# Kernel optimization log

Hardware: AMD Instinct MI355X
Metric: run time of the kernel (lower is better)

## Reference

```python
import jax, jax.numpy as jnp
import numpy as np
import math

H = 8          # n_head
MAX_POS = 48   # block_size / max_positions
MAX_PART = 16  # max_particles


def _rel_bias(table, L, max_len):
    # table: (2*max_len-1, H). Equivalent to the tile/view trick in
    # SimpleRelativePositionalBias: bias[h, i, j] = b[j - i + L - 1, h]
    b = table[max_len - L: max_len + L - 1]          # (2L-1, H)
    idx = jnp.arange(L)
    rel = idx[None, :] - idx[:, None] + (L - 1)      # (L, L) in [0, 2L-2]
    return jnp.transpose(b[rel], (2, 0, 1))          # (H, L, L)


def setup_inputs() -> dict:
    key = jax.random.key(0)
    ks = jax.random.split(key, 7)
    B, N, T, C = 16, 16, 48, 512
    s = 0.02
    return {
        "x": jax.random.normal(ks[0], (B, N, T, C), jnp.float32),
        "Wq": jax.random.normal(ks[1], (C, C), jnp.float32) * s,
        "Wk": jax.random.normal(ks[2], (C, C), jnp.float32) * s,
        "Wv": jax.random.normal(ks[3], (C, C), jnp.float32) * s,
        "Wo": jax.random.normal(ks[4], (C, C), jnp.float32) * s,
        "rel_pos_bias": jax.random.normal(ks[5], (2 * MAX_POS - 1, H), jnp.float32) * s,
        "particle_rel_pos_bias": jax.random.normal(ks[6], (2 * MAX_PART - 1, H), jnp.float32) * s,
    }


def reference(x, Wq, Wk, Wv, Wo, rel_pos_bias, particle_rel_pos_bias):
    B, N, T, C = x.shape
    hd = C // H
    L = N * T
    xf = x.reshape(B, L, C)
    # (B, H, L, hd) each; Linear with no bias
    q = (xf @ Wq).reshape(B, L, H, hd).transpose(0, 2, 1, 3)
    k = (xf @ Wk).reshape(B, L, H, hd).transpose(0, 2, 1, 3)
    v = (xf @ Wv).reshape(B, L, H, hd).transpose(0, 2, 1, 3)

    att = jnp.einsum('bhqd,bhkd->bhqk', q, k) * (1.0 / math.sqrt(hd))
    att = att.reshape(B, H, N, T, N, T)

    bias_t = _rel_bias(rel_pos_bias, T, MAX_POS).reshape(1, H, 1, T, 1, T)
    bias_p = _rel_bias(particle_rel_pos_bias, N, MAX_PART).reshape(1, H, N, 1, N, 1)
    att = att + bias_t + bias_p

    # causal over the time axes only (all particles at allowed times visible)
    causal = jnp.tril(jnp.ones((T, T), dtype=bool))
    att = jnp.where(causal[None, None, None, :, None, :], att, -jnp.inf)

    att = jax.nn.softmax(att.reshape(B, H, L, L), axis=-1)
    y = att @ v                                      # (B, H, L, hd)
    y = y.transpose(0, 2, 1, 3).reshape(B, L, C) @ Wo
    return y.reshape(B, N, T, C)
```

## Files before the change

### kernel.cpp

```cpp
#include <hip/hip_runtime.h>
#include <hip/hip_bf16.h>
#include <math.h>

#define B_  16
#define N_  16
#define T_  48
#define C_  512
#define H_  8
#define HD_ 64
#define L_  768
#define BL_ 12288

typedef __attribute__((ext_vector_type(8))) short b16x8;
typedef __attribute__((ext_vector_type(4))) float f32x4;
typedef __attribute__((ext_vector_type(2))) unsigned int u32x2;

__device__ __forceinline__ short f2b(float f) {
  __hip_bfloat16 h = __float2bfloat16(f);
  return *reinterpret_cast<short*>(&h);
}
__device__ __forceinline__ unsigned cvt_pk_bf16(float a, float b) {
  unsigned d;
  asm("v_cvt_pk_bf16_f32 %0, %1, %2" : "=v"(d) : "v"(a), "v"(b));
  return d;
}
__device__ __forceinline__ float ex2(float x) {
  float d;
  asm("v_exp_f32 %0, %1" : "=v"(d) : "v"(x));
  return d;
}
__device__ __forceinline__ void gload16(const void* g, void* l) {
  __builtin_amdgcn_global_load_lds(
      (const __attribute__((address_space(1))) void*)g,
      (__attribute__((address_space(3))) void*)l, 16, 0, 0);
}

__global__ __launch_bounds__(256) void prep_kernel(
    const float* __restrict__ x,
    const float* __restrict__ Wq, const float* __restrict__ Wk,
    const float* __restrict__ Wv, const float* __restrict__ Wo,
    short* __restrict__ xb, short* __restrict__ WT)
{
  __shared__ float tile[32][33];
  int blk = blockIdx.x;
  int tid = threadIdx.x;
  if (blk < 3072) {
    int i = blk * 256 + tid;
    const float4* src = (const float4*)(x + (size_t)i * 8);
    float4 a = src[0], b = src[1];
    short tmp[8] = {f2b(a.x), f2b(a.y), f2b(a.z), f2b(a.w),
                    f2b(b.x), f2b(b.y), f2b(b.z), f2b(b.w)};
    *(b16x8*)(xb + (size_t)i * 8) = *(b16x8*)tmp;
  } else {
    int idx = blk - 3072;
    int mat = idx >> 8, rem = idx & 255;
    const float* W = (mat == 0) ? Wq : (mat == 1) ? Wk : (mat == 2) ? Wv : Wo;
    float scale = (mat == 0) ? 0.18033688f : 1.0f;
    int k0 = (rem >> 4) * 32, n0 = (rem & 15) * 32;
    int tx = tid & 31, ty = tid >> 5;
    for (int i = ty; i < 32; i += 8) tile[i][tx] = W[(size_t)(k0 + i) * 512 + n0 + tx];
    __syncthreads();
    short* dst = WT + (size_t)mat * 262144;
    for (int i = ty; i < 32; i += 8)
      dst[(size_t)(n0 + i) * 512 + k0 + tx] = f2b(tile[tx][i] * scale);
  }
}

__global__ __launch_bounds__(256) void qkv_kernel(
    const short* __restrict__ xb, const short* __restrict__ WT,
    short* __restrict__ q2, short* __restrict__ k2, short* __restrict__ vT2)
{
  __shared__ __align__(16) short smem[16384];
  int tid = threadIdx.x;
  int w = tid >> 6, lane = tid & 63, n16 = lane & 15, quad = lane >> 4;
  int bm = blockIdx.x, bn = blockIdx.y;
  int mat = bn >> 2;
  int ncol0 = (bn & 3) * 128;
  const short* Wt = WT + (size_t)mat * 262144;
  int bq = bm / 6;
  int rr0 = (bm % 6) * 128;

  f32x4 zero4 = {0.f, 0.f, 0.f, 0.f};
  f32x4 acc[4][4];
  #pragma unroll
  for (int mt = 0; mt < 4; ++mt)
    #pragma unroll
    for (int nt = 0; nt < 4; ++nt) acc[mt][nt] = zero4;

  const short* gA[2];
  const short* gB[2];
  #pragma unroll
  for (int i = 0; i < 2; ++i) {
    int r16 = w + 4 * i;
    int rr = rr0 + r16 * 16 + (lane >> 2);
    int pt = rr >> 4, pn = rr & 15;
    gA[i] = xb + ((size_t)bq * 768 + pn * 48 + pt) * 512 + (lane & 3) * 8;
    gB[i] = Wt + (size_t)(ncol0 + r16 * 16 + (lane >> 2)) * 512 + (lane & 3) * 8;
  }
  int ldsoff = (w) * 512 + lane * 8;

  auto stage = [&](int buf, int kt) {
    short* As = smem + buf * 8192;
    short* Bs = As + 4096;
    #pragma unroll
    for (int i = 0; i < 2; ++i) {
      gload16(gA[i] + kt * 32, As + i * 2048 + ldsoff);
      gload16(gB[i] + kt * 32, Bs + i * 2048 + ldsoff);
    }
  };

  int wm = (w >> 1) * 64, wn = (w & 1) * 64;
  stage(0, 0);
  __syncthreads();
  int buf = 0;
  for (int kt = 0; kt < 16; ++kt) {
    if (kt < 15) stage(buf ^ 1, kt + 1);
    const short (*As)[32] = (const short(*)[32])(smem + buf * 8192);
    const short (*Bs)[32] = (const short(*)[32])(smem + buf * 8192 + 4096);
    b16x8 af[4], bf[4];
    #pragma unroll
    for (int mt = 0; mt < 4; ++mt) af[mt] = *(const b16x8*)&As[wm + mt * 16 + n16][quad * 8];
    #pragma unroll
    for (int nt = 0; nt < 4; ++nt) bf[nt] = *(const b16x8*)&Bs[wn + nt * 16 + n16][quad * 8];
    #pragma unroll
    for (int mt = 0; mt < 4; ++mt)
      #pragma unroll
      for (int nt = 0; nt < 4; ++nt)
        acc[mt][nt] = __builtin_amdgcn_mfma_f32_16x16x32_bf16(af[mt], bf[nt], acc[mt][nt], 0, 0, 0);
    __syncthreads();
    buf ^= 1;
  }

  short (*Ls)[136] = (short(*)[136])smem;
  for (int c = 0; c < 4; ++c) {
    __syncthreads();
    if ((w >> 1) == (c >> 1)) {
      int mtb = (c & 1) * 2;
      #pragma unroll
      for (int mi = 0; mi < 2; ++mi) {
        #pragma unroll
        for (int nt = 0; nt < 4; ++nt)
          #pragma unroll
          for (int r = 0; r < 4; ++r)
            Ls[mi * 16 + quad * 4 + r][wn + nt * 16 + n16] = f2b(acc[mtb + mi][nt][r]);
      }
    }
    __syncthreads();
    int rrc = rr0 + c * 32;
    if (mat != 2) {
      short* dst = (mat == 0) ? q2 : k2;
      int row = tid >> 3, c0 = (tid & 7) * 16;
      int hhg = (ncol0 + c0) >> 6, d0 = (ncol0 + c0) & 63;
      short* dp = dst + ((size_t)(bq * 8 + hhg) * 768 + rrc + row) * 64 + d0;
      *(b16x8*)dp       = *(b16x8*)&Ls[row][c0];
      *(b16x8*)(dp + 8) = *(b16x8*)&Ls[row][c0 + 8];
    } else {
      int cp = tid & 63, r8 = (tid >> 6) * 8;
      int c0 = 2 * cp;
      int hhg = (ncol0 + c0) >> 6, d0 = (ncol0 + c0) & 63;
      short t0[8], t1[8];
      #pragma unroll
      for (int j = 0; j < 8; ++j) { t0[j] = Ls[r8 + j][c0]; t1[j] = Ls[r8 + j][c0 + 1]; }
      short* dp = vT2 + ((size_t)(bq * 8 + hhg) * 64 + d0) * 768 + rrc + r8;
      *(b16x8*)dp         = *(b16x8*)t0;
      *(b16x8*)(dp + 768) = *(b16x8*)t1;
    }
  }
}

__global__ __launch_bounds__(128, 3) void attn_kernel(
    const short* __restrict__ q2, const short* __restrict__ k2,
    const short* __restrict__ vT2,
    const float* __restrict__ relT, const float* __restrict__ relP,
    short* __restrict__ yatt)
{
  __shared__ __align__(16) short KV[2][4096];
  __shared__ float btL[2][96];

  const float LOG2E = 1.44269504f;
  int tid = threadIdx.x;
  int wv = tid >> 6, lane = tid & 63, n16 = lane & 15, quad = lane >> 4;
  int blk = blockIdx.x;
  int h = blk & 7;
  int g = blk >> 3;
  int pg = g % 12, b = g / 12;
  int pair = pg * 2 + wv;
  int qtA = pair, qtB = 47 - pair;
  int nA = pg + 1;
  int nB = 24 - pg;

  btL[wv][lane] = relT[(lane < 95 ? lane : 94) * 8 + h] * LOG2E;
  if (lane < 32) btL[wv][64 + lane] = relT[((64 + lane) < 95 ? 64 + lane : 94) * 8 + h] * LOG2E;

  float bpT[4];
  #pragma unroll
  for (int r = 0; r < 4; ++r)
    bpT[r] = relP[(quad * 4 + r - n16 + 15) * 8 + h] * LOG2E;

  size_t bh = (size_t)(b * 8 + h);
  const short* qb = q2 + bh * 49152;
  const short* kb = k2 + bh * 49152;
  const short* vb = vT2 + bh * 49152;

  b16x8 qA0 = *(const b16x8*)(qb + (qtA * 16 + n16) * 64 + quad * 8);
  b16x8 qA1 = *(const b16x8*)(qb + (qtA * 16 + n16) * 64 + quad * 8 + 32);
  b16x8 qB0 = *(const b16x8*)(qb + (qtB * 16 + n16) * 64 + quad * 8);
  b16x8 qB1 = *(const b16x8*)(qb + (qtB * 16 + n16) * 64 + quad * 8 + 32);

  f32x4 zero4 = {0.f, 0.f, 0.f, 0.f};
  f32x4 oA[4], oB[4];
  float psA = 0.f, psB = 0.f;
  #pragma unroll
  for (int nt = 0; nt < 4; ++nt) { oA[nt] = zero4; oB[nt] = zero4; }

  int krow = tid >> 3, kc8 = tid & 7;
  int vd   = tid >> 2, vkc = tid & 3;
  int kdst = (kc8 < 4 ? 0 : 1024) + krow * 32 + (kc8 & 3) * 8;
  int vdst = 2048 + vd * 32 + vkc * 8;
  b16x8 s0, s1, s2, s3;
  auto LOADR = [&](int kt2) {
    const short* kq = kb + (size_t)(kt2 * 32 + krow) * 64 + kc8 * 8;
    s0 = *(const b16x8*)kq;
    s1 = *(const b16x8*)(kq + 16 * 64);
    const short* vq = vb + (size_t)vd * 768 + kt2 * 32 + vkc * 8;
    s2 = *(const b16x8*)vq;
    s3 = *(const b16x8*)(vq + (size_t)32 * 768);
  };
  auto WRITE = [&](int buf) {
    short* p = KV[buf];
    *(b16x8*)(p + kdst)       = s0;
    *(b16x8*)(p + kdst + 512) = s1;
    *(b16x8*)(p + vdst)        = s2;
    *(b16x8*)(p + vdst + 1024) = s3;
  };

  auto exp_pack = [&](const f32x4& s0v, const f32x4& s1v, float bt0, float bt1,
                      float& ps) -> b16x8 {
    float e00 = ex2(s0v[0] + bt0 + bpT[0]);
    float e01 = ex2(s0v[1] + bt0 + bpT[1]);
    float e02 = ex2(s0v[2] + bt0 + bpT[2]);
    float e03 = ex2(s0v[3] + bt0 + bpT[3]);
    float e10 = ex2(s1v[0] + bt1 + bpT[0]);
    float e11 = ex2(s1v[1] + bt1 + bpT[1]);
    float e12 = ex2(s1v[2] + bt1 + bpT[2]);
    float e13 = ex2(s1v[3] + bt1 + bpT[3]);
    ps += ((e00 + e01) + (e02 + e03)) + ((e10 + e11) + (e12 + e13));
    unsigned p0 = cvt_pk_bf16(e00, e01);
    unsigned p1 = cvt_pk_bf16(e02, e03);
    unsigned p2 = cvt_pk_bf16(e10, e11);
    unsigned p3 = cvt_pk_bf16(e12, e13);
    u32x2 a02 = __builtin_amdgcn_permlane32_swap(p0, p2, false, false);
    u32x2 z02 = __builtin_amdgcn_permlane16_swap(a02.x, a02.y, false, false);
    u32x2 a13 = __builtin_amdgcn_permlane32_swap(p1, p3, false, false);
    u32x2 z13 = __builtin_amdgcn_permlane16_swap(a13.x, a13.y, false, false);
    union { unsigned u[4]; b16x8 v; } r;
    r.u[0] = z02.x;
    r.u[1] = z13.x;
    r.u[2] = z02.y;
    r.u[3] = z13.y;
    return r.v;
  };

  LOADR(0);
  WRITE(0);
  __syncthreads();

  int buf = 0;
  for (int kt2 = 0; kt2 < nB; ++kt2) {
    bool more = (kt2 + 1 < nB);
    if (more) LOADR(kt2 + 1);

    const short* p = KV[buf];
    b16x8 kf0 = *(const b16x8*)(p + n16 * 32 + quad * 8);
    b16x8 kf1 = *(const b16x8*)(p + 1024 + n16 * 32 + quad * 8);
    b16x8 kf2 = *(const b16x8*)(p + (16 + n16) * 32 + quad * 8);
    b16x8 kf3 = *(const b16x8*)(p + 1024 + (16 + n16) * 32 + quad * 8);
    b16x8 vf0 = *(const b16x8*)(p + 2048 + n16 * 32 + quad * 8);
    b16x8 vf1 = *(const b16x8*)(p + 2048 + (16 + n16) * 32 + quad * 8);
    b16x8 vf2 = *(const b16x8*)(p + 2048 + (32 + n16) * 32 + quad * 8);
    b16x8 vf3 = *(const b16x8*)(p + 2048 + (48 + n16) * 32 + quad * 8);

    int kt0 = kt2 * 2;
    bool doA = kt2 < nA;
    f32x4 sB0 = zero4, sB1 = zero4;
    sB0 = __builtin_amdgcn_mfma_f32_16x16x32_bf16(kf0, qB0, sB0, 0, 0, 0);
    sB0 = __builtin_amdgcn_mfma_f32_16x16x32_bf16(kf1, qB1, sB0, 0, 0, 0);
    sB1 = __builtin_amdgcn_mfma_f32_16x16x32_bf16(kf2, qB0, sB1, 0, 0, 0);
    sB1 = __builtin_amdgcn_mfma_f32_16x16x32_bf16(kf3, qB1, sB1, 0, 0, 0);
    f32x4 sA0 = zero4, sA1 = zero4;
    if (doA) {
      sA0 = __builtin_amdgcn_mfma_f32_16x16x32_bf16(kf0, qA0, sA0, 0, 0, 0);
      sA0 = __builtin_amdgcn_mfma_f32_16x16x32_bf16(kf1, qA1, sA0, 0, 0, 0);
      sA1 = __builtin_amdgcn_mfma_f32_16x16x32_bf16(kf2, qA0, sA1, 0, 0, 0);
      sA1 = __builtin_amdgcn_mfma_f32_16x16x32_bf16(kf3, qA1, sA1, 0, 0, 0);
    }
    float btB0 = (kt0 <= qtB) ? btL[wv][kt0 - qtB + 47] : -1e30f;
    float btB1 = (kt0 + 1 <= qtB) ? btL[wv][kt0 + 1 - qtB + 47] : -1e30f;
    b16x8 pfB = exp_pack(sB0, sB1, btB0, btB1, psB);
    oB[0] = __builtin_amdgcn_mfma_f32_16x16x32_bf16(pfB, vf0, oB[0], 0, 0, 0);
    oB[1] = __builtin_amdgcn_mfma_f32_16x16x32_bf16(pfB, vf1, oB[1], 0, 0, 0);
    oB[2] = __builtin_amdgcn_mfma_f32_16x16x32_bf16(pfB, vf2, oB[2], 0, 0, 0);
    oB[3] = __builtin_amdgcn_mfma_f32_16x16x32_bf16(pfB, vf3, oB[3], 0, 0, 0);
    if (doA) {
      float btA0 = (kt0 <= qtA) ? btL[wv][kt0 - qtA + 47] : -1e30f;
      float btA1 = (kt0 + 1 <= qtA) ? btL[wv][kt0 + 1 - qtA + 47] : -1e30f;
      b16x8 pfA = exp_pack(sA0, sA1, btA0, btA1, psA);
      oA[0] = __builtin_amdgcn_mfma_f32_16x16x32_bf16(pfA, vf0, oA[0], 0, 0, 0);
      oA[1] = __builtin_amdgcn_mfma_f32_16x16x32_bf16(pfA, vf1, oA[1], 0, 0, 0);
      oA[2] = __builtin_amdgcn_mfma_f32_16x16x32_bf16(pfA, vf2, oA[2], 0, 0, 0);
      oA[3] = __builtin_amdgcn_mfma_f32_16x16x32_bf16(pfA, vf3, oA[3], 0, 0, 0);
    }

    if (more) WRITE(buf ^ 1);
    __syncthreads();
    buf ^= 1;
  }

  psA += __shfl_xor(psA, 16); psA += __shfl_xor(psA, 32);
  psB += __shfl_xor(psB, 16); psB += __shfl_xor(psB, 32);
  float invA = 1.0f / psA, invB = 1.0f / psB;
  float pnA[4], pnB[4];
  #pragma unroll
  for (int r = 0; r < 4; ++r) {
    pnA[r] = __shfl(invA, quad * 4 + r);
    pnB[r] = __shfl(invB, quad * 4 + r);
  }

  #pragma unroll
  for (int nt = 0; nt < 4; ++nt) {
    int c = h * 64 + nt * 16 + n16;
    #pragma unroll
    for (int r = 0; r < 4; ++r) {
      int qn = quad * 4 + r;
      yatt[((size_t)b * 768 + qn * 48 + qtA) * 512 + c] = f2b(oA[nt][r] * pnA[r]);
      yatt[((size_t)b * 768 + qn * 48 + qtB) * 512 + c] = f2b(oB[nt][r] * pnB[r]);
    }
  }
}

__global__ __launch_bounds__(256) void proj_kernel(
    const short* __restrict__ yatt, const short* __restrict__ WT,
    float* __restrict__ out)
{
  __shared__ __align__(16) short smem[16384];
  int tid = threadIdx.x;
  int w = tid >> 6, lane = tid & 63, n16 = lane & 15, quad = lane >> 4;
  int row0 = blockIdx.x * 128;
  int ncol0 = blockIdx.y * 128;
  const short* Wt = WT + (size_t)3 * 262144;

  f32x4 zero4 = {0.f, 0.f, 0.f, 0.f};
  f32x4 acc[4][4];
  #pragma unroll
  for (int mt = 0; mt < 4; ++mt)
    #pragma unroll
    for (int nt = 0; nt < 4; ++nt) acc[mt][nt] = zero4;

  const short* gA[2];
  const short* gB[2];
  #pragma unroll
  for (int i = 0; i < 2; ++i) {
    int r16 = w + 4 * i;
    gA[i] = yatt + (size_t)(row0 + r16 * 16 + (lane >> 2)) * 512 + (lane & 3) * 8;
    gB[i] = Wt + (size_t)(ncol0 + r16 * 16 + (lane >> 2)) * 512 + (lane & 3) * 8;
  }
  int ldsoff = w * 512 + lane * 8;

  auto stage = [&](int buf, int kt) {
    short* As = smem + buf * 8192;
    short* Bs = As + 4096;
    #pragma unroll
    for (int i = 0; i < 2; ++i) {
      gload16(gA[i] + kt * 32, As + i * 2048 + ldsoff);
      gload16(gB[i] + kt * 32, Bs + i * 2048 + ldsoff);
    }
  };

  int wm = (w >> 1) * 64, wn = (w & 1) * 64;
  stage(0, 0);
  __syncthreads();
  int buf = 0;
  for (int kt = 0; kt < 16; ++kt) {
    if (kt < 15) stage(buf ^ 1, kt + 1);
    const short (*As)[32] = (const short(*)[32])(smem + buf * 8192);
    const short (*Bs)[32] = (const short(*)[32])(smem + buf * 8192 + 4096);
    b16x8 af[4], bf[4];
    #pragma unroll
    for (int mt = 0; mt < 4; ++mt) af[mt] = *(const b16x8*)&As[wm + mt * 16 + n16][quad * 8];
    #pragma unroll
    for (int nt = 0; nt < 4; ++nt) bf[nt] = *(const b16x8*)&Bs[wn + nt * 16 + n16][quad * 8];
    #pragma unroll
    for (int mt = 0; mt < 4; ++mt)
      #pragma unroll
      for (int nt = 0; nt < 4; ++nt)
        acc[mt][nt] = __builtin_amdgcn_mfma_f32_16x16x32_bf16(af[mt], bf[nt], acc[mt][nt], 0, 0, 0);
    __syncthreads();
    buf ^= 1;
  }

  #pragma unroll
  for (int mt = 0; mt < 4; ++mt) {
    int rowb = row0 + wm + mt * 16 + quad * 4;
    #pragma unroll
    for (int nt = 0; nt < 4; ++nt) {
      int colg = ncol0 + wn + nt * 16 + n16;
      #pragma unroll
      for (int r = 0; r < 4; ++r)
        out[(size_t)(rowb + r) * 512 + colg] = acc[mt][nt][r];
    }
  }
}

extern "C" void kernel_launch(void* const* d_in, const int* in_sizes, int n_in,
                              void* d_out, int out_size, void* d_ws, size_t ws_size,
                              hipStream_t stream) {
  const float* x    = (const float*)d_in[0];
  const float* Wq   = (const float*)d_in[1];
  const float* Wk   = (const float*)d_in[2];
  const float* Wv   = (const float*)d_in[3];
  const float* Wo   = (const float*)d_in[4];
  const float* relT = (const float*)d_in[5];
  const float* relP = (const float*)d_in[6];

  char* wsb = (char*)d_ws;
  const size_t SZ = (size_t)BL_ * C_ * 2;
  short* xb  = (short*)(wsb);
  short* WT  = (short*)(wsb + SZ);
  short* qb  = (short*)(wsb + SZ + 2097152);
  short* kb  = (short*)(wsb + 2 * SZ + 2097152);
  short* vTb = (short*)(wsb + 3 * SZ + 2097152);
  short* yat = (short*)(wsb + 4 * SZ + 2097152 + 4096);

  prep_kernel<<<dim3(4096), dim3(256), 0, stream>>>(x, Wq, Wk, Wv, Wo, xb, WT);
  qkv_kernel<<<dim3(96, 12), dim3(256), 0, stream>>>(xb, WT, qb, kb, vTb);
  attn_kernel<<<dim3(1536), dim3(128), 0, stream>>>(qb, kb, vTb, relT, relP, yat);
  proj_kernel<<<dim3(96, 4), dim3(256), 0, stream>>>(yat, WT, (float*)d_out);
}
```

Before: 157.4 us.

## Share K/V tiles across four waves per block and add MFMA priority hints

The attention kernel now runs 256-thread blocks with four waves, each handling a pair of query tiles, so every K/V tile staged in shared memory is reused by twice as many waves. Grid size is halved and each thread loads half as much per stage. Each wave skips compute once it passes its own causal limit, but it keeps joining the block barriers. s_setprio is placed around the MFMA groups to favour matrix issue. The trade-off is load imbalance inside a block, since waves with shorter causal ranges sit idle until the longest wave finishes.

```diff
diff --git a/kernel.cpp b/kernel.cpp
--- a/kernel.cpp
+++ b/kernel.cpp
@@ -168,29 +168,29 @@
   }
 }
 
-__global__ __launch_bounds__(128, 3) void attn_kernel(
+__global__ __launch_bounds__(256, 4) void attn_kernel(
     const short* __restrict__ q2, const short* __restrict__ k2,
     const short* __restrict__ vT2,
     const float* __restrict__ relT, const float* __restrict__ relP,
     short* __restrict__ yatt)
 {
   __shared__ __align__(16) short KV[2][4096];
-  __shared__ float btL[2][96];
+  __shared__ float btL[96];
 
   const float LOG2E = 1.44269504f;
   int tid = threadIdx.x;
-  int wv = tid >> 6, lane = tid & 63, n16 = lane & 15, quad = lane >> 4;
+  int w = tid >> 6, lane = tid & 63, n16 = lane & 15, quad = lane >> 4;
   int blk = blockIdx.x;
   int h = blk & 7;
   int g = blk >> 3;
-  int pg = g % 12, b = g / 12;
-  int pair = pg * 2 + wv;
-  int qtA = pair, qtB = 47 - pair;
-  int nA = pg + 1;
-  int nB = 24 - pg;
-
-  btL[wv][lane] = relT[(lane < 95 ? lane : 94) * 8 + h] * LOG2E;
-  if (lane < 32) btL[wv][64 + lane] = relT[((64 + lane) < 95 ? 64 + lane : 94) * 8 + h] * LOG2E;
+  int pgg = g % 6, b = g / 6;
+  int pairq = pgg * 4 + w;
+  int qtA = pairq, qtB = 47 - pairq;
+  int nAw = (qtA + 2) >> 1;
+  int nBw = (qtB + 2) >> 1;
+  int nBmax = 24 - 2 * pgg;
+
+  if (tid < 96) btL[tid] = relT[(tid < 95 ? tid : 94) * 8 + h] * LOG2E;
 
   float bpT[4];
   #pragma unroll
@@ -217,21 +217,14 @@
   int vd   = tid >> 2, vkc = tid & 3;
   int kdst = (kc8 < 4 ? 0 : 1024) + krow * 32 + (kc8 & 3) * 8;
   int vdst = 2048 + vd * 32 + vkc * 8;
-  b16x8 s0, s1, s2, s3;
+  b16x8 s0, s2;
   auto LOADR = [&](int kt2) {
-    const short* kq = kb + (size_t)(kt2 * 32 + krow) * 64 + kc8 * 8;
-    s0 = *(const b16x8*)kq;
-    s1 = *(const b16x8*)(kq + 16 * 64);
-    const short* vq = vb + (size_t)vd * 768 + kt2 * 32 + vkc * 8;
-    s2 = *(const b16x8*)vq;
-    s3 = *(const b16x8*)(vq + (size_t)32 * 768);
+    s0 = *(const b16x8*)(kb + (size_t)(kt2 * 32 + krow) * 64 + kc8 * 8);
+    s2 = *(const b16x8*)(vb + (size_t)vd * 768 + kt2 * 32 + vkc * 8);
   };
   auto WRITE = [&](int buf) {
-    short* p = KV[buf];
-    *(b16x8*)(p + kdst)       = s0;
-    *(b16x8*)(p + kdst + 512) = s1;
-    *(b16x8*)(p + vdst)        = s2;
-    *(b16x8*)(p + vdst + 1024) = s3;
+    *(b16x8*)(KV[buf] + kdst) = s0;
+    *(b16x8*)(KV[buf] + vdst) = s2;
   };
 
   auto exp_pack = [&](const f32x4& s0v, const f32x4& s1v, float bt0, float bt1,
@@ -266,49 +259,58 @@
   __syncthreads();
 
   int buf = 0;
-  for (int kt2 = 0; kt2 < nB; ++kt2) {
-    bool more = (kt2 + 1 < nB);
+  for (int kt2 = 0; kt2 < nBmax; ++kt2) {
+    bool more = (kt2 + 1 < nBmax);
     if (more) LOADR(kt2 + 1);
 
-    const short* p = KV[buf];
-    b16x8 kf0 = *(const b16x8*)(p + n16 * 32 + quad * 8);
-    b16x8 kf1 = *(const b16x8*)(p + 1024 + n16 * 32 + quad * 8);
-    b16x8 kf2 = *(const b16x8*)(p + (16 + n16) * 32 + quad * 8);
-    b16x8 kf3 = *(const b16x8*)(p + 1024 + (16 + n16) * 32 + quad * 8);
-    b16x8 vf0 = *(const b16x8*)(p + 2048 + n16 * 32 + quad * 8);
-    b16x8 vf1 = *(const b16x8*)(p + 2048 + (16 + n16) * 32 + quad * 8);
-    b16x8 vf2 = *(const b16x8*)(p + 2048 + (32 + n16) * 32 + quad * 8);
-    b16x8 vf3 = *(const b16x8*)(p + 2048 + (48 + n16) * 32 + quad * 8);
-
-    int kt0 = kt2 * 2;
-    bool doA = kt2 < nA;
-    f32x4 sB0 = zero4, sB1 = zero4;
-    sB0 = __builtin_amdgcn_mfma_f32_16x16x32_bf16(kf0, qB0, sB0, 0, 0, 0);
-    sB0 = __builtin_amdgcn_mfma_f32_16x16x32_bf16(kf1, qB1, sB0, 0, 0, 0);
-    sB1 = __builtin_amdgcn_mfma_f32_16x16x32_bf16(kf2, qB0, sB1, 0, 0, 0);
-    sB1 = __builtin_amdgcn_mfma_f32_16x16x32_bf16(kf3, qB1, sB1, 0, 0, 0);
-    f32x4 sA0 = zero4, sA1 = zero4;
-    if (doA) {
-      sA0 = __builtin_amdgcn_mfma_f32_16x16x32_bf16(kf0, qA0, sA0, 0, 0, 0);
-      sA0 = __builtin_amdgcn_mfma_f32_16x16x32_bf16(kf1, qA1, sA0, 0, 0, 0);
-      sA1 = __builtin_amdgcn_mfma_f32_16x16x32_bf16(kf2, qA0, sA1, 0, 0, 0);
-      sA1 = __builtin_amdgcn_mfma_f32_16x16x32_bf16(kf3, qA1, sA1, 0, 0, 0);
-    }
-    float btB0 = (kt0 <= qtB) ? btL[wv][kt0 - qtB + 47] : -1e30f;
-    float btB1 = (kt0 + 1 <= qtB) ? btL[wv][kt0 + 1 - qtB + 47] : -1e30f;
-    b16x8 pfB = exp_pack(sB0, sB1, btB0, btB1, psB);
-    oB[0] = __builtin_amdgcn_mfma_f32_16x16x32_bf16(pfB, vf0, oB[0], 0, 0, 0);
-    oB[1] = __builtin_amdgcn_mfma_f32_16x16x32_bf16(pfB, vf1, oB[1], 0, 0, 0);
-    oB[2] = __builtin_amdgcn_mfma_f32_16x16x32_bf16(pfB, vf2, oB[2], 0, 0, 0);
-    oB[3] = __builtin_amdgcn_mfma_f32_16x16x32_bf16(pfB, vf3, oB[3], 0, 0, 0);
-    if (doA) {
-      float btA0 = (kt0 <= qtA) ? btL[wv][kt0 - qtA + 47] : -1e30f;
-      float btA1 = (kt0 + 1 <= qtA) ? btL[wv][kt0 + 1 - qtA + 47] : -1e30f;
-      b16x8 pfA = exp_pack(sA0, sA1, btA0, btA1, psA);
-      oA[0] = __builtin_amdgcn_mfma_f32_16x16x32_bf16(pfA, vf0, oA[0], 0, 0, 0);
-      oA[1] = __builtin_amdgcn_mfma_f32_16x16x32_bf16(pfA, vf1, oA[1], 0, 0, 0);
-      oA[2] = __builtin_amdgcn_mfma_f32_16x16x32_bf16(pfA, vf2, oA[2], 0, 0, 0);
-      oA[3] = __builtin_amdgcn_mfma_f32_16x16x32_bf16(pfA, vf3, oA[3], 0, 0, 0);
+    bool doB = kt2 < nBw;
+    bool doA = kt2 < nAw;
+    if (doB) {
+      const short* p = KV[buf];
+      b16x8 kf0 = *(const b16x8*)(p + n16 * 32 + quad * 8);
+      b16x8 kf1 = *(const b16x8*)(p + 1024 + n16 * 32 + quad * 8);
+      b16x8 kf2 = *(const b16x8*)(p + (16 + n16) * 32 + quad * 8);
+      b16x8 kf3 = *(const b16x8*)(p + 1024 + (16 + n16) * 32 + quad * 8);
+      b16x8 vf0 = *(const b16x8*)(p + 2048 + n16 * 32 + quad * 8);
+      b16x8 vf1 = *(const b16x8*)(p + 2048 + (16 + n16) * 32 + quad * 8);
+      b16x8 vf2 = *(const b16x8*)(p + 2048 + (32 + n16) * 32 + quad * 8);
+      b16x8 vf3 = *(const b16x8*)(p + 2048 + (48 + n16) * 32 + quad * 8);
+
+      int kt0 = kt2 * 2;
+      __builtin_amdgcn_s_setprio(1);
+      f32x4 sB0 = zero4, sB1 = zero4;
+      sB0 = __builtin_amdgcn_mfma_f32_16x16x32_bf16(kf0, qB0, sB0, 0, 0, 0);
+      sB0 = __builtin_amdgcn_mfma_f32_16x16x32_bf16(kf1, qB1, sB0, 0, 0, 0);
+      sB1 = __builtin_amdgcn_mfma_f32_16x16x32_bf16(kf2, qB0, sB1, 0, 0, 0);
+      sB1 = __builtin_amdgcn_mfma_f32_16x16x32_bf16(kf3, qB1, sB1, 0, 0, 0);
+      f32x4 sA0 = zero4, sA1 = zero4;
+      if (doA) {
+        sA0 = __builtin_amdgcn_mfma_f32_16x16x32_bf16(kf0, qA0, sA0, 0, 0, 0);
+        sA0 = __builtin_amdgcn_mfma_f32_16x16x32_bf16(kf1, qA1, sA0, 0, 0, 0);
+        sA1 = __builtin_amdgcn_mfma_f32_16x16x32_bf16(kf2, qA0, sA1, 0, 0, 0);
+        sA1 = __builtin_amdgcn_mfma_f32_16x16x32_bf16(kf3, qA1, sA1, 0, 0, 0);
+      }
+      __builtin_amdgcn_s_setprio(0);
+      float btB0 = (kt0 <= qtB) ? btL[kt0 - qtB + 47] : -1e30f;
+      float btB1 = (kt0 + 1 <= qtB) ? btL[kt0 + 1 - qtB + 47] : -1e30f;
+      b16x8 pfB = exp_pack(sB0, sB1, btB0, btB1, psB);
+      __builtin_amdgcn_s_setprio(1);
+      oB[0] = __builtin_amdgcn_mfma_f32_16x16x32_bf16(pfB, vf0, oB[0], 0, 0, 0);
+      oB[1] = __builtin_amdgcn_mfma_f32_16x16x32_bf16(pfB, vf1, oB[1], 0, 0, 0);
+      oB[2] = __builtin_amdgcn_mfma_f32_16x16x32_bf16(pfB, vf2, oB[2], 0, 0, 0);
+      oB[3] = __builtin_amdgcn_mfma_f32_16x16x32_bf16(pfB, vf3, oB[3], 0, 0, 0);
+      __builtin_amdgcn_s_setprio(0);
+      if (doA) {
+        float btA0 = (kt0 <= qtA) ? btL[kt0 - qtA + 47] : -1e30f;
+        float btA1 = (kt0 + 1 <= qtA) ? btL[kt0 + 1 - qtA + 47] : -1e30f;
+        b16x8 pfA = exp_pack(sA0, sA1, btA0, btA1, psA);
+        __builtin_amdgcn_s_setprio(1);
+        oA[0] = __builtin_amdgcn_mfma_f32_16x16x32_bf16(pfA, vf0, oA[0], 0, 0, 0);
+        oA[1] = __builtin_amdgcn_mfma_f32_16x16x32_bf16(pfA, vf1, oA[1], 0, 0, 0);
+        oA[2] = __builtin_amdgcn_mfma_f32_16x16x32_bf16(pfA, vf2, oA[2], 0, 0, 0);
+        oA[3] = __builtin_amdgcn_mfma_f32_16x16x32_bf16(pfA, vf3, oA[3], 0, 0, 0);
+        __builtin_amdgcn_s_setprio(0);
+      }
     }
 
     if (more) WRITE(buf ^ 1);
@@ -433,6 +435,6 @@
 
   prep_kernel<<<dim3(4096), dim3(256), 0, stream>>>(x, Wq, Wk, Wv, Wo, xb, WT);
   qkv_kernel<<<dim3(96, 12), dim3(256), 0, stream>>>(xb, WT, qb, kb, vTb);
-  attn_kernel<<<dim3(1536), dim3(128), 0, stream>>>(qb, kb, vTb, relT, relP, yat);
+  attn_kernel<<<dim3(768), dim3(256), 0, stream>>>(qb, kb, vTb, relT, relP, yat);
   proj_kernel<<<dim3(96, 4), dim3(256), 0, stream>>>(yat, WT, (float*)d_out);
 }
```

New measurement: 156.9 us, median of 2. No clear change (-0.3%).

## Process four query time-tiles per wave to reuse K/V fragments

Applied to the files above, without the earlier changes.

Each wave in the attention kernel now handles two pairs of causally-balanced query time tiles (four in total) instead of one pair. Each K/V tile loaded into LDS and registers is therefore reused across more queries, and the grid shrinks from 1536 to 768 blocks. The relative-bias table is shared between the waves instead of duplicated per wave. In exchange it roughly doubles accumulator and Q register use, lowers the occupancy hint from 3 to 2, and within a block the two waves can now have unequal amounts of work.

```diff
diff --git a/kernel.cpp b/kernel.cpp
--- a/kernel.cpp
+++ b/kernel.cpp
@@ -168,29 +168,30 @@
   }
 }
 
-__global__ __launch_bounds__(128, 3) void attn_kernel(
+__global__ __launch_bounds__(128, 2) void attn_kernel(
     const short* __restrict__ q2, const short* __restrict__ k2,
     const short* __restrict__ vT2,
     const float* __restrict__ relT, const float* __restrict__ relP,
     short* __restrict__ yatt)
 {
   __shared__ __align__(16) short KV[2][4096];
-  __shared__ float btL[2][96];
+  __shared__ float btL[96];
 
   const float LOG2E = 1.44269504f;
   int tid = threadIdx.x;
-  int wv = tid >> 6, lane = tid & 63, n16 = lane & 15, quad = lane >> 4;
+  int w = tid >> 6, lane = tid & 63, n16 = lane & 15, quad = lane >> 4;
   int blk = blockIdx.x;
   int h = blk & 7;
   int g = blk >> 3;
-  int pg = g % 12, b = g / 12;
-  int pair = pg * 2 + wv;
-  int qtA = pair, qtB = 47 - pair;
-  int nA = pg + 1;
-  int nB = 24 - pg;
-
-  btL[wv][lane] = relT[(lane < 95 ? lane : 94) * 8 + h] * LOG2E;
-  if (lane < 32) btL[wv][64 + lane] = relT[((64 + lane) < 95 ? 64 + lane : 94) * 8 + h] * LOG2E;
+  int pgg = g % 6, b = g / 6;
+  int base = pgg * 4 + 2 * w;
+  int qtA0 = base,     qtB0 = 47 - base;
+  int qtA1 = base + 1, qtB1 = 46 - base;
+  int nA0 = (qtA0 + 2) >> 1, nA1 = (qtA1 + 2) >> 1;
+  int nB0 = (qtB0 + 2) >> 1, nB1 = (qtB1 + 2) >> 1;
+  int nBmax = 24 - 2 * pgg;
+
+  if (tid < 96) btL[tid] = relT[(tid < 95 ? tid : 94) * 8 + h] * LOG2E;
 
   float bpT[4];
   #pragma unroll
@@ -202,16 +203,22 @@
   const short* kb = k2 + bh * 49152;
   const short* vb = vT2 + bh * 49152;
 
-  b16x8 qA0 = *(const b16x8*)(qb + (qtA * 16 + n16) * 64 + quad * 8);
-  b16x8 qA1 = *(const b16x8*)(qb + (qtA * 16 + n16) * 64 + quad * 8 + 32);
-  b16x8 qB0 = *(const b16x8*)(qb + (qtB * 16 + n16) * 64 + quad * 8);
-  b16x8 qB1 = *(const b16x8*)(qb + (qtB * 16 + n16) * 64 + quad * 8 + 32);
+  b16x8 qA0_0 = *(const b16x8*)(qb + (qtA0 * 16 + n16) * 64 + quad * 8);
+  b16x8 qA0_1 = *(const b16x8*)(qb + (qtA0 * 16 + n16) * 64 + quad * 8 + 32);
+  b16x8 qA1_0 = *(const b16x8*)(qb + (qtA1 * 16 + n16) * 64 + quad * 8);
+  b16x8 qA1_1 = *(const b16x8*)(qb + (qtA1 * 16 + n16) * 64 + quad * 8 + 32);
+  b16x8 qB0_0 = *(const b16x8*)(qb + (qtB0 * 16 + n16) * 64 + quad * 8);
+  b16x8 qB0_1 = *(const b16x8*)(qb + (qtB0 * 16 + n16) * 64 + quad * 8 + 32);
+  b16x8 qB1_0 = *(const b16x8*)(qb + (qtB1 * 16 + n16) * 64 + quad * 8);
+  b16x8 qB1_1 = *(const b16x8*)(qb + (qtB1 * 16 + n16) * 64 + quad * 8 + 32);
 
   f32x4 zero4 = {0.f, 0.f, 0.f, 0.f};
-  f32x4 oA[4], oB[4];
-  float psA = 0.f, psB = 0.f;
-  #pragma unroll
-  for (int nt = 0; nt < 4; ++nt) { oA[nt] = zero4; oB[nt] = zero4; }
+  f32x4 oA0[4], oA1[4], oB0[4], oB1[4];
+  float psA0 = 0.f, psA1 = 0.f, psB0 = 0.f, psB1 = 0.f;
+  #pragma unroll
+  for (int nt = 0; nt < 4; ++nt) {
+    oA0[nt] = zero4; oA1[nt] = zero4; oB0[nt] = zero4; oB1[nt] = zero4;
+  }
 
   int krow = tid >> 3, kc8 = tid & 7;
   int vd   = tid >> 2, vkc = tid & 3;
@@ -228,8 +235,8 @@
   };
   auto WRITE = [&](int buf) {
     short* p = KV[buf];
-    *(b16x8*)(p + kdst)       = s0;
-    *(b16x8*)(p + kdst + 512) = s1;
+    *(b16x8*)(p + kdst)        = s0;
+    *(b16x8*)(p + kdst + 512)  = s1;
     *(b16x8*)(p + vdst)        = s2;
     *(b16x8*)(p + vdst + 1024) = s3;
   };
@@ -261,54 +268,71 @@
     return r.v;
   };
 
+  auto qk = [&](const b16x8* kf, const b16x8& q0, const b16x8& q1,
+                f32x4& sv0, f32x4& sv1) {
+    sv0 = zero4; sv1 = zero4;
+    sv0 = __builtin_amdgcn_mfma_f32_16x16x32_bf16(kf[0], q0, sv0, 0, 0, 0);
+    sv0 = __builtin_amdgcn_mfma_f32_16x16x32_bf16(kf[1], q1, sv0, 0, 0, 0);
+    sv1 = __builtin_amdgcn_mfma_f32_16x16x32_bf16(kf[2], q0, sv1, 0, 0, 0);
+    sv1 = __builtin_amdgcn_mfma_f32_16x16x32_bf16(kf[3], q1, sv1, 0, 0, 0);
+  };
+  auto pv = [&](const b16x8& pf, const b16x8* vf, f32x4* o) {
+    o[0] = __builtin_amdgcn_mfma_f32_16x16x32_bf16(pf, vf[0], o[0], 0, 0, 0);
+    o[1] = __builtin_amdgcn_mfma_f32_16x16x32_bf16(pf, vf[1], o[1], 0, 0, 0);
+    o[2] = __builtin_amdgcn_mfma_f32_16x16x32_bf16(pf, vf[2], o[2], 0, 0, 0);
+    o[3] = __builtin_amdgcn_mfma_f32_16x16x32_bf16(pf, vf[3], o[3], 0, 0, 0);
+  };
+
   LOADR(0);
   WRITE(0);
   __syncthreads();
 
   int buf = 0;
-  for (int kt2 = 0; kt2 < nB; ++kt2) {
-    bool more = (kt2 + 1 < nB);
+  for (int kt2 = 0; kt2 < nBmax; ++kt2) {
+    bool more = (kt2 + 1 < nBmax);
     if (more) LOADR(kt2 + 1);
 
+    bool dB0 = kt2 < nB0, dB1 = kt2 < nB1;
+    bool dA1 = kt2 < nA1, dA0 = kt2 < nA0;
     const short* p = KV[buf];
-    b16x8 kf0 = *(const b16x8*)(p + n16 * 32 + quad * 8);
-    b16x8 kf1 = *(const b16x8*)(p + 1024 + n16 * 32 + quad * 8);
-    b16x8 kf2 = *(const b16x8*)(p + (16 + n16) * 32 + quad * 8);
-    b16x8 kf3 = *(const b16x8*)(p + 1024 + (16 + n16) * 32 + quad * 8);
-    b16x8 vf0 = *(const b16x8*)(p + 2048 + n16 * 32 + quad * 8);
-    b16x8 vf1 = *(const b16x8*)(p + 2048 + (16 + n16) * 32 + quad * 8);
-    b16x8 vf2 = *(const b16x8*)(p + 2048 + (32 + n16) * 32 + quad * 8);
-    b16x8 vf3 = *(const b16x8*)(p + 2048 + (48 + n16) * 32 + quad * 8);
-
-    int kt0 = kt2 * 2;
-    bool doA = kt2 < nA;
-    f32x4 sB0 = zero4, sB1 = zero4;
-    sB0 = __builtin_amdgcn_mfma_f32_16x16x32_bf16(kf0, qB0, sB0, 0, 0, 0);
-    sB0 = __builtin_amdgcn_mfma_f32_16x16x32_bf16(kf1, qB1, sB0, 0, 0, 0);
-    sB1 = __builtin_amdgcn_mfma_f32_16x16x32_bf16(kf2, qB0, sB1, 0, 0, 0);
-    sB1 = __builtin_amdgcn_mfma_f32_16x16x32_bf16(kf3, qB1, sB1, 0, 0, 0);
-    f32x4 sA0 = zero4, sA1 = zero4;
-    if (doA) {
-      sA0 = __builtin_amdgcn_mfma_f32_16x16x32_bf16(kf0, qA0, sA0, 0, 0, 0);
-      sA0 = __builtin_amdgcn_mfma_f32_16x16x32_bf16(kf1, qA1, sA0, 0, 0, 0);
-      sA1 = __builtin_amdgcn_mfma_f32_16x16x32_bf16(kf2, qA0, sA1, 0, 0, 0);
-      sA1 = __builtin_amdgcn_mfma_f32_16x16x32_bf16(kf3, qA1, sA1, 0, 0, 0);
-    }
-    float btB0 = (kt0 <= qtB) ? btL[wv][kt0 - qtB + 47] : -1e30f;
-    float btB1 = (kt0 + 1 <= qtB) ? btL[wv][kt0 + 1 - qtB + 47] : -1e30f;
-    b16x8 pfB = exp_pack(sB0, sB1, btB0, btB1, psB);
-    oB[0] = __builtin_amdgcn_mfma_f32_16x16x32_bf16(pfB, vf0, oB[0], 0, 0, 0);
-    oB[1] = __builtin_amdgcn_mfma_f32_16x16x32_bf16(pfB, vf1, oB[1], 0, 0, 0);
-    oB[2] = __builtin_amdgcn_mfma_f32_16x16x32_bf16(pfB, vf2, oB[2], 0, 0, 0);
-    oB[3] = __builtin_amdgcn_mfma_f32_16x16x32_bf16(pfB, vf3, oB[3], 0, 0, 0);
-    if (doA) {
-      float btA0 = (kt0 <= qtA) ? btL[wv][kt0 - qtA + 47] : -1e30f;
-      float btA1 = (kt0 + 1 <= qtA) ? btL[wv][kt0 + 1 - qtA + 47] : -1e30f;
-      b16x8 pfA = exp_pack(sA0, sA1, btA0, btA1, psA);
-      oA[0] = __builtin_amdgcn_mfma_f32_16x16x32_bf16(pfA, vf0, oA[0], 0, 0, 0);
-      oA[1] = __builtin_amdgcn_mfma_f32_16x16x32_bf16(pfA, vf1, oA[1], 0, 0, 0);
-      oA[2] = __builtin_amdgcn_mfma_f32_16x16x32_bf16(pfA, vf2, oA[2], 0, 0, 0);
-      oA[3] = __builtin_amdgcn_mfma_f32_16x16x32_bf16(pfA, vf3, oA[3], 0, 0, 0);
+    b16x8 kf[4], vf[4];
+    if (dB0) {
+      kf[0] = *(const b16x8*)(p + n16 * 32 + quad * 8);
+      kf[1] = *(const b16x8*)(p + 1024 + n16 * 32 + quad * 8);
+      kf[2] = *(const b16x8*)(p + (16 + n16) * 32 + quad * 8);
+      kf[3] = *(const b16x8*)(p + 1024 + (16 + n16) * 32 + quad * 8);
+      vf[0] = *(const b16x8*)(p + 2048 + n16 * 32 + quad * 8);
+      vf[1] = *(const b16x8*)(p + 2048 + (16 + n16) * 32 + quad * 8);
+      vf[2] = *(const b16x8*)(p + 2048 + (32 + n16) * 32 + quad * 8);
+      vf[3] = *(const b16x8*)(p + 2048 + (48 + n16) * 32 + quad * 8);
+
+      int kt0 = kt2 * 2;
+      f32x4 sB0a, sB0b, sB1a, sB1b, sA0a, sA0b, sA1a, sA1b;
+      qk(kf, qB0_0, qB0_1, sB0a, sB0b);
+      if (dB1) qk(kf, qB1_0, qB1_1, sB1a, sB1b);
+      if (dA1) qk(kf, qA1_0, qA1_1, sA1a, sA1b);
+      if (dA0) qk(kf, qA0_0, qA0_1, sA0a, sA0b);
+
+      {
+        float bt0 = (kt0 <= qtB0) ? btL[kt0 - qtB0 + 47] : -1e30f;
+        float bt1 = (kt0 + 1 <= qtB0) ? btL[kt0 + 1 - qtB0 + 47] : -1e30f;
+        pv(exp_pack(sB0a, sB0b, bt0, bt1, psB0), vf, oB0);
+      }
+      if (dB1) {
+        float bt0 = (kt0 <= qtB1) ? btL[kt0 - qtB1 + 47] : -1e30f;
+        float bt1 = (kt0 + 1 <= qtB1) ? btL[kt0 + 1 - qtB1 + 47] : -1e30f;
+        pv(exp_pack(sB1a, sB1b, bt0, bt1, psB1), vf, oB1);
+      }
+      if (dA1) {
+        float bt0 = (kt0 <= qtA1) ? btL[kt0 - qtA1 + 47] : -1e30f;
+        float bt1 = (kt0 + 1 <= qtA1) ? btL[kt0 + 1 - qtA1 + 47] : -1e30f;
+        pv(exp_pack(sA1a, sA1b, bt0, bt1, psA1), vf, oA1);
+      }
+      if (dA0) {
+        float bt0 = (kt0 <= qtA0) ? btL[kt0 - qtA0 + 47] : -1e30f;
+        float bt1 = (kt0 + 1 <= qtA0) ? btL[kt0 + 1 - qtA0 + 47] : -1e30f;
+        pv(exp_pack(sA0a, sA0b, bt0, bt1, psA0), vf, oA0);
+      }
     }
 
     if (more) WRITE(buf ^ 1);
@@ -316,26 +340,27 @@
     buf ^= 1;
   }
 
-  psA += __shfl_xor(psA, 16); psA += __shfl_xor(psA, 32);
-  psB += __shfl_xor(psB, 16); psB += __shfl_xor(psB, 32);
-  float invA = 1.0f / psA, invB = 1.0f / psB;
-  float pnA[4], pnB[4];
-  #pragma unroll
-  for (int r = 0; r < 4; ++r) {
-    pnA[r] = __shfl(invA, quad * 4 + r);
-    pnB[r] = __shfl(invB, quad * 4 + r);
-  }
-
-  #pragma unroll
-  for (int nt = 0; nt < 4; ++nt) {
-    int c = h * 64 + nt * 16 + n16;
-    #pragma unroll
-    for (int r = 0; r < 4; ++r) {
-      int qn = quad * 4 + r;
-      yatt[((size_t)b * 768 + qn * 48 + qtA) * 512 + c] = f2b(oA[nt][r] * pnA[r]);
-      yatt[((size_t)b * 768 + qn * 48 + qtB) * 512 + c] = f2b(oB[nt][r] * pnB[r]);
-    }
-  }
+  auto finish = [&](float ps, f32x4* o, int qt) {
+    ps += __shfl_xor(ps, 16);
+    ps += __shfl_xor(ps, 32);
+    float inv = 1.0f / ps;
+    float pn[4];
+    #pragma unroll
+    for (int r = 0; r < 4; ++r) pn[r] = __shfl(inv, quad * 4 + r);
+    #pragma unroll
+    for (int nt = 0; nt < 4; ++nt) {
+      int c = h * 64 + nt * 16 + n16;
+      #pragma unroll
+      for (int r = 0; r < 4; ++r) {
+        int qn = quad * 4 + r;
+        yatt[((size_t)b * 768 + qn * 48 + qt) * 512 + c] = f2b(o[nt][r] * pn[r]);
+      }
+    }
+  };
+  finish(psB0, oB0, qtB0);
+  finish(psB1, oB1, qtB1);
+  finish(psA1, oA1, qtA1);
+  finish(psA0, oA0, qtA0);
 }
 
 __global__ __launch_bounds__(256) void proj_kernel(
@@ -433,6 +458,6 @@
 
   prep_kernel<<<dim3(4096), dim3(256), 0, stream>>>(x, Wq, Wk, Wv, Wo, xb, WT);
   qkv_kernel<<<dim3(96, 12), dim3(256), 0, stream>>>(xb, WT, qb, kb, vTb);
-  attn_kernel<<<dim3(1536), dim3(128), 0, stream>>>(qb, kb, vTb, relT, relP, yat);
+  attn_kernel<<<dim3(768), dim3(128), 0, stream>>>(qb, kb, vTb, relT, relP, yat);
   proj_kernel<<<dim3(96, 4), dim3(256), 0, stream>>>(yat, WT, (float*)d_out);
 }
```

Result: slower. 160.6 us (+2.0%).
